# Kernel optimization log

Measured on AMD Instinct MI355X. Metric: run time of the kernel, lower is better.

## Reference

```python
import jax, jax.numpy as jnp
import numpy as np

DIM = 512
NUM_HEADS = 16
RANK = 4
HEAD_DIM = DIM // NUM_HEADS
SCALE = HEAD_DIM ** -0.5
B_, N, NW = 2048, 49, 64


def setup_inputs() -> dict:
    key = jax.random.key(0)
    ks = jax.random.split(key, 9)
    x = jax.random.normal(ks[0], (B_, N, DIM), dtype=jnp.float32)
    mask = jax.random.normal(ks[1], (NW, N, N), dtype=jnp.float32)
    # qkv base linear (torch Linear stores weight [out,in])
    W_qkv = jax.random.normal(ks[2], (3 * DIM, DIM), dtype=jnp.float32) * (DIM ** -0.5)
    b_qkv = jax.random.normal(ks[3], (3 * DIM,), dtype=jnp.float32) * 0.02
    # LoRA down [rank, dim], up [3*dim, rank] (zero-init in module; use small random for non-trivial math)
    A_down = jax.random.normal(ks[4], (RANK, DIM), dtype=jnp.float32) * 0.02
    B_up = jax.random.normal(ks[5], (3 * DIM, RANK), dtype=jnp.float32) * 0.02
    W_proj = jax.random.normal(ks[6], (DIM, DIM), dtype=jnp.float32) * (DIM ** -0.5)
    b_proj = jax.random.normal(ks[7], (DIM,), dtype=jnp.float32) * 0.02
    return {"x": x, "mask": mask, "W_qkv": W_qkv, "b_qkv": b_qkv,
            "A_down": A_down, "B_up": B_up, "W_proj": W_proj, "b_proj": b_proj}


def reference(x, mask, W_qkv, b_qkv, A_down, B_up, W_proj, b_proj):
    Bw, n, C = x.shape
    H, hd = NUM_HEADS, HEAD_DIM
    # LoRA-augmented QKV projection: base linear + up(down(x))
    qkv = x @ W_qkv.T + b_qkv + (x @ A_down.T) @ B_up.T          # [B_, N, 3C]
    qkv = qkv.reshape(Bw, n, 3, H, hd)
    q = qkv[:, :, 0].transpose(0, 2, 1, 3)                        # [B_, H, N, hd]
    k = qkv[:, :, 1].transpose(0, 2, 1, 3)
    v = qkv[:, :, 2].transpose(0, 2, 1, 3)
    attn = jnp.einsum('bhnd,bhmd->bhnm', q, k) * SCALE            # [B_, H, N, N]
    nW = mask.shape[0]
    attn = attn.reshape(Bw // nW, nW, H, n, n) + mask[None, :, None]
    attn = attn.reshape(Bw, H, n, n)
    attn = jax.nn.softmax(attn, axis=-1)
    out = jnp.einsum('bhnm,bhmd->bhnd', attn, v)                  # [B_, H, N, hd]
    out = out.transpose(0, 2, 1, 3).reshape(Bw, n, C)
    return out @ W_proj.T + b_proj
```

## Files before the change

kernel.cpp:

```cpp
#include <hip/hip_runtime.h>
#include <stdint.h>

typedef __attribute__((ext_vector_type(4))) float f32x4;
typedef __attribute__((ext_vector_type(8))) __bf16 bf16x8;
typedef __attribute__((ext_vector_type(4))) unsigned int u32x4;
typedef __attribute__((ext_vector_type(4))) unsigned short u16x4;

#define TOK 49
#define NHEAD 16
#define HDIM 32
#define CDIM 512
#define NB 2048
#define MTOT (NB * TOK)
#define ATT_SCALE 0.17677669529663687f

__device__ __forceinline__ unsigned short f2bf(float f) {
  return __builtin_bit_cast(unsigned short, (__bf16)f);
}

__device__ __forceinline__ void gl_lds16(const void* g, const void* lds) {
  __builtin_amdgcn_global_load_lds(
      (__attribute__((address_space(1))) void*)(uintptr_t)g,
      (__attribute__((address_space(3))) void*)(uint32_t)(uintptr_t)lds,
      16, 0, 0);
}

__device__ __forceinline__ f32x4 mfma16(bf16x8 a, bf16x8 b, f32x4 c) {
  return __builtin_amdgcn_mfma_f32_16x16x32_bf16(a, b, c, 0, 0, 0);
}

__global__ __launch_bounds__(256) void k_prep_weff(
    const float* __restrict__ Wqkv, const float* __restrict__ Bup,
    const float* __restrict__ Adown, unsigned short* __restrict__ weff) {
  int idx = blockIdx.x * 256 + threadIdx.x;
  if (idx >= 3 * CDIM * CDIM) return;
  int o = idx >> 9, i = idx & 511;
  float v = Wqkv[idx];
#pragma unroll
  for (int r = 0; r < 4; r++) v += Bup[o * 4 + r] * Adown[r * 512 + i];
  weff[idx] = f2bf(v);
}

__global__ __launch_bounds__(256) void k_conv4(
    const float* __restrict__ src, unsigned short* __restrict__ dst, int n4) {
  for (int i = blockIdx.x * blockDim.x + threadIdx.x; i < n4;
       i += gridDim.x * blockDim.x) {
    f32x4 v = *(const f32x4*)(src + (size_t)i * 4);
    u16x4 o;
    o[0] = f2bf(v[0]); o[1] = f2bf(v[1]); o[2] = f2bf(v[2]); o[3] = f2bf(v[3]);
    *(u16x4*)(dst + (size_t)i * 4) = o;
  }
}

template <int NT, bool SPLIT>
__global__ __launch_bounds__(256, 2) void k_gemmW(
    const unsigned short* __restrict__ A, const unsigned short* __restrict__ Bw,
    const float* __restrict__ bias,
    unsigned short* __restrict__ qo, unsigned short* __restrict__ ko,
    unsigned short* __restrict__ vo, float* __restrict__ fo) {
  __shared__ __attribute__((aligned(16))) unsigned short smem[36864];
  const int t = threadIdx.x;
  const int l = t & 63;
  const int l15 = l & 15, lq = l >> 4;
  const int w = t >> 6;
  const int wr = w >> 1, wc = w & 1;
  const int bid = blockIdx.x;
  const int lb = (bid & 7) * ((int)gridDim.x >> 3) + (bid >> 3);
  const int mt = lb / NT, nt = lb % NT;
  const size_t m0 = (size_t)mt * 128;
  const int n0 = nt * 256;

  auto stage = [&](int kt, int bb) {
    unsigned short* dA = smem + bb * 4096;
#pragma unroll
    for (int q = 0; q < 2; ++q) {
      const int li = q * 256 + t;
      const int row = li >> 2, sl = li & 3;
      gl_lds16(A + (m0 + row) * CDIM + kt * 32 + ((sl ^ ((row >> 1) & 3)) << 3),
               &dA[li * 8]);
    }
    unsigned short* dB = smem + 12288 + bb * 8192;
#pragma unroll
    for (int q = 0; q < 4; ++q) {
      const int li = q * 256 + t;
      const int row = li >> 2, sl = li & 3;
      gl_lds16(Bw + (size_t)(n0 + row) * CDIM + kt * 32 +
                   ((sl ^ ((row >> 1) & 3)) << 3),
               &dB[li * 8]);
    }
  };

  f32x4 acc[4][8] = {};
  stage(0, 0);
  stage(1, 1);
  for (int kt = 0; kt < 16; ++kt) {
    const int cur = kt % 3;
    if (kt < 15) {
      asm volatile("s_waitcnt vmcnt(6)" ::: "memory");
    } else {
      asm volatile("s_waitcnt vmcnt(0)" ::: "memory");
    }
    __builtin_amdgcn_s_barrier();
    asm volatile("" ::: "memory");
    if (kt < 14) stage(kt + 2, (kt + 2) % 3);
    const unsigned short* bufA = smem + cur * 4096;
    const unsigned short* bufB = smem + 12288 + cur * 8192;
    bf16x8 af[4], bfv[8];
#pragma unroll
    for (int f = 0; f < 4; ++f) {
      const int r = wr * 64 + f * 16 + l15;
      af[f] = __builtin_bit_cast(
          bf16x8, *(const u32x4*)&bufA[r * 32 + ((lq ^ ((r >> 1) & 3)) << 3)]);
    }
#pragma unroll
    for (int c = 0; c < 8; ++c) {
      const int r = wc * 128 + c * 16 + l15;
      bfv[c] = __builtin_bit_cast(
          bf16x8, *(const u32x4*)&bufB[r * 32 + ((lq ^ ((r >> 1) & 3)) << 3)]);
    }
    __builtin_amdgcn_s_setprio(1);
#pragma unroll
    for (int f = 0; f < 4; ++f) {
#pragma unroll
      for (int c = 0; c < 8; ++c) acc[f][c] = mfma16(af[f], bfv[c], acc[f][c]);
    }
    __builtin_amdgcn_s_setprio(0);
    asm volatile("" ::: "memory");
  }

  __syncthreads();
  if constexpr (SPLIT) {
    unsigned short* ep = smem + w * 8192;
#pragma unroll
    for (int J = 0; J < 8; ++J) {
      const int colb = n0 + wc * 128 + J * 16 + l15;
      const float bv = bias[colb];
      const int sl0 = J * 2 + (l15 >> 3);
#pragma unroll
      for (int I = 0; I < 4; ++I) {
#pragma unroll
        for (int r = 0; r < 4; ++r) {
          const int row = I * 16 + lq * 4 + r;
          ep[row * 128 + ((sl0 ^ (row & 7)) << 3) + (l15 & 7)] =
              f2bf(acc[I][J][r] + bv);
        }
      }
    }
    asm volatile("s_waitcnt lgkmcnt(0)" ::: "memory");
    __builtin_amdgcn_s_barrier();
#pragma unroll
    for (int rnd = 0; rnd < 16; ++rnd) {
      const int sub = rnd * 16 + (l >> 2);
      const int mloc = sub >> 2, hd = sub & 3;
      const int colh = n0 + wc * 128 + hd * 32;
      const int which = colh >> 9;
      const int hh = (colh >> 5) & 15;
      unsigned short* dst = which == 0 ? qo : (which == 1 ? ko : vo);
      const uint32_t mg = (uint32_t)(m0 + wr * 64 + mloc);
      const uint32_t bw_ = mg / 49u;
      const uint32_t nn = mg - bw_ * 49u;
      const int slot = hd * 4 + (l & 3);
      u32x4 v = *(const u32x4*)&ep[mloc * 128 + ((slot ^ (mloc & 7)) << 3)];
      *(u32x4*)&dst[((size_t)(bw_ * 16u + hh) * 49u + nn) * 32u + (l & 3) * 8] =
          v;
    }
  } else {
    float* ep32 = (float*)(smem) + w * 4096;
#pragma unroll
    for (int ch = 0; ch < 2; ++ch) {
#pragma unroll
      for (int J2 = 0; J2 < 4; ++J2) {
        const int colb = n0 + wc * 128 + ch * 64 + J2 * 16 + l15;
        const float bv = bias[colb];
        const int sl0 = J2 * 4 + (l15 >> 2);
#pragma unroll
        for (int I = 0; I < 4; ++I) {
#pragma unroll
          for (int r = 0; r < 4; ++r) {
            const int row = I * 16 + lq * 4 + r;
            ep32[row * 64 + ((sl0 ^ (row & 7)) << 2) + (l15 & 3)] =
                acc[I][ch * 4 + J2][r] + bv;
          }
        }
      }
      asm volatile("s_waitcnt lgkmcnt(0)" ::: "memory");
#pragma unroll
      for (int rnd = 0; rnd < 16; ++rnd) {
        const int row = rnd * 4 + (l >> 4);
        const int slot = l & 15;
        f32x4 v = *(const f32x4*)&ep32[row * 64 + ((slot ^ (row & 7)) << 2)];
        const size_t mg = m0 + wr * 64 + row;
        *(f32x4*)&fo[mg * CDIM + n0 + wc * 128 + ch * 64 + (l & 15) * 4] = v;
      }
      asm volatile("s_waitcnt lgkmcnt(0)" ::: "memory");
      asm volatile("" ::: "memory");
    }
  }
}

__global__ __launch_bounds__(256) void k_attn(
    const unsigned short* __restrict__ qb, const unsigned short* __restrict__ kb,
    const unsigned short* __restrict__ vb, const float* __restrict__ mask,
    unsigned short* __restrict__ ao) {
  __shared__ __attribute__((aligned(16))) unsigned short sP[4][64 * 64];
  __shared__ __attribute__((aligned(16))) unsigned short sV[4][32 * 64];
  const int t = threadIdx.x;
  const int l = t & 63, w = t >> 6;
  const int l15 = l & 15, lq = l >> 4;
  const int pair = blockIdx.x * 4 + w;
  const int b = pair >> 4, h = pair & 15;
  const size_t base = (size_t)pair * (TOK * HDIM);
  unsigned short* P = sP[w];
  unsigned short* Vt = sV[w];

  bf16x8 qf[4], kf[4];
#pragma unroll
  for (int i = 0; i < 4; i++)
    qf[i] = __builtin_bit_cast(
        bf16x8, *(const u32x4*)(qb + base + (size_t)(i * 16 + l15) * 32 + lq * 8));
#pragma unroll
  for (int i = 0; i < 4; i++)
    kf[i] = __builtin_bit_cast(
        bf16x8, *(const u32x4*)(kb + base + (size_t)(i * 16 + l15) * 32 + lq * 8));
  u32x4 vr[4];
#pragma unroll
  for (int j = 0; j < 4; j++)
    vr[j] = *(const u32x4*)(vb + base + (size_t)l * 32 + j * 8);

  f32x4 s[4][4];
  __builtin_amdgcn_s_setprio(1);
#pragma unroll
  for (int i = 0; i < 4; i++) {
#pragma unroll
    for (int j = 0; j < 4; j++) s[i][j] = mfma16(qf[i], kf[j], (f32x4)0.0f);
  }
  __builtin_amdgcn_s_setprio(0);

  const bool vok = (l < TOK);
  const int tsl = ((l >> 3) & 7);
  const int tlo = l & 7;
#pragma unroll
  for (int j = 0; j < 4; j++) {
#pragma unroll
    for (int c = 0; c < 4; c++) {
      uint32_t u = vr[j][c];
      int d0 = j * 8 + c * 2;
      Vt[(d0 + 0) * 64 + ((tsl ^ ((d0 + 0) & 7)) << 3) + tlo] =
          vok ? (unsigned short)(u & 0xFFFFu) : (unsigned short)0;
      Vt[(d0 + 1) * 64 + ((tsl ^ ((d0 + 1) & 7)) << 3) + tlo] =
          vok ? (unsigned short)(u >> 16) : (unsigned short)0;
    }
  }

  const float* mrow = mask + (size_t)(b & 63) * (TOK * TOK);
#pragma unroll
  for (int i = 0; i < 4; i++) {
#pragma unroll
    for (int r = 0; r < 4; r++) {
      int row = i * 16 + lq * 4 + r;
#pragma unroll
      for (int j = 0; j < 4; j++) {
        int col = j * 16 + l15;
        float xv = s[i][j][r] * ATT_SCALE;
        if (col < TOK) {
          if (row < TOK) xv += mrow[row * TOK + col];
        } else {
          xv = -1e30f;
        }
        s[i][j][r] = xv;
      }
    }
  }

  float rinv[4][4];
#pragma unroll
  for (int i = 0; i < 4; i++) {
#pragma unroll
    for (int r = 0; r < 4; r++) {
      float m = fmaxf(fmaxf(s[i][0][r], s[i][1][r]), fmaxf(s[i][2][r], s[i][3][r]));
      m = fmaxf(m, __shfl_xor(m, 1));
      m = fmaxf(m, __shfl_xor(m, 2));
      m = fmaxf(m, __shfl_xor(m, 4));
      m = fmaxf(m, __shfl_xor(m, 8));
      float sum = 0.f;
      int row = i * 16 + lq * 4 + r;
#pragma unroll
      for (int j = 0; j < 4; j++) {
        float p = __expf(s[i][j][r] - m);
        sum += p;
        P[row * 64 + (((j * 2 + (l15 >> 3)) ^ (row & 7)) << 3) + (l15 & 7)] =
            f2bf(p);
      }
      sum += __shfl_xor(sum, 1);
      sum += __shfl_xor(sum, 2);
      sum += __shfl_xor(sum, 4);
      sum += __shfl_xor(sum, 8);
      rinv[i][r] = 1.0f / sum;
    }
  }

  asm volatile("s_waitcnt lgkmcnt(0)" ::: "memory");
  __builtin_amdgcn_sched_barrier(0);

  f32x4 o[4][2] = {};
#pragma unroll
  for (int ks = 0; ks < 2; ks++) {
    bf16x8 pa[4], vf[2];
#pragma unroll
    for (int i = 0; i < 4; i++)
      pa[i] = __builtin_bit_cast(
          bf16x8,
          *(const u32x4*)&P[(i * 16 + l15) * 64 + (((lq + ks * 4) ^ (l15 & 7)) << 3)]);
#pragma unroll
    for (int j = 0; j < 2; j++)
      vf[j] = __builtin_bit_cast(
          bf16x8,
          *(const u32x4*)&Vt[(j * 16 + l15) * 64 + (((lq + ks * 4) ^ (l15 & 7)) << 3)]);
    __builtin_amdgcn_s_setprio(1);
#pragma unroll
    for (int i = 0; i < 4; i++) {
#pragma unroll
      for (int j = 0; j < 2; j++) o[i][j] = mfma16(pa[i], vf[j], o[i][j]);
    }
    __builtin_amdgcn_s_setprio(0);
  }

#pragma unroll
  for (int i = 0; i < 4; i++) {
#pragma unroll
    for (int r = 0; r < 4; r++) {
      int row = i * 16 + lq * 4 + r;
      if (row < TOK) {
        float inv = rinv[i][r];
        size_t obase = ((size_t)b * TOK + row) * CDIM + h * HDIM;
#pragma unroll
        for (int j = 0; j < 2; j++)
          ao[obase + j * 16 + l15] = f2bf(o[i][j][r] * inv);
      }
    }
  }
}

extern "C" void kernel_launch(void* const* d_in, const int* in_sizes, int n_in,
                              void* d_out, int out_size, void* d_ws,
                              size_t ws_size, hipStream_t stream) {
  const float* x = (const float*)d_in[0];
  const float* mask = (const float*)d_in[1];
  const float* Wqkv = (const float*)d_in[2];
  const float* bqkv = (const float*)d_in[3];
  const float* Adown = (const float*)d_in[4];
  const float* Bup = (const float*)d_in[5];
  const float* Wproj = (const float*)d_in[6];
  const float* bproj = (const float*)d_in[7];
  float* out = (float*)d_out;
  char* ws = (char*)d_ws;

  size_t off = 0;
  auto alloc = [&](size_t bytes) {
    size_t o = off;
    off += (bytes + 255) & ~(size_t)255;
    return o;
  };
  const size_t qkv_elems = (size_t)NB * NHEAD * TOK * HDIM;
  unsigned short* weff = (unsigned short*)(ws + alloc((size_t)3 * CDIM * CDIM * 2));
  unsigned short* wpb = (unsigned short*)(ws + alloc((size_t)CDIM * CDIM * 2));
  unsigned short* qb = (unsigned short*)(ws + alloc(qkv_elems * 2 + 4096));
  unsigned short* kb = (unsigned short*)(ws + alloc(qkv_elems * 2 + 4096));
  unsigned short* vb = (unsigned short*)(ws + alloc(qkv_elems * 2 + 4096));
  unsigned short* xb = (unsigned short*)(ws + alloc((size_t)MTOT * CDIM * 2));
  unsigned short* ao = xb;

  k_prep_weff<<<(3 * CDIM * CDIM + 255) / 256, 256, 0, stream>>>(Wqkv, Bup,
                                                                 Adown, weff);
  k_conv4<<<256, 256, 0, stream>>>(Wproj, wpb, CDIM * CDIM / 4);
  k_conv4<<<2048, 256, 0, stream>>>(x, xb, MTOT * CDIM / 4);
  k_gemmW<6, true><<<(MTOT / 128) * 6, 256, 0, stream>>>(
      xb, weff, bqkv, qb, kb, vb, nullptr);
  k_attn<<<NB * NHEAD / 4, 256, 0, stream>>>(qb, kb, vb, mask, ao);
  k_gemmW<2, false><<<(MTOT / 128) * 2, 256, 0, stream>>>(
      ao, wpb, bproj, nullptr, nullptr, nullptr, out);
}
```

Before: 541.5 us.

## Fuse fp32-to-bf16 x conversion into QKV GEMM and stage mask in LDS

```diff
diff --git a/kernel.cpp b/kernel.cpp
--- a/kernel.cpp
+++ b/kernel.cpp
@@ -16,6 +16,9 @@
 
 __device__ __forceinline__ unsigned short f2bf(float f) {
   return __builtin_bit_cast(unsigned short, (__bf16)f);
+}
+__device__ __forceinline__ float bf2f(unsigned short u) {
+  return __builtin_bit_cast(float, (uint32_t)u << 16);
 }
 
 __device__ __forceinline__ void gl_lds16(const void* g, const void* lds) {
@@ -52,13 +55,16 @@
   }
 }
 
-template <int NT, bool SPLIT>
-__global__ __launch_bounds__(256, 2) void k_gemmW(
-    const unsigned short* __restrict__ A, const unsigned short* __restrict__ Bw,
+template <int NT, bool SPLIT, bool AF32>
+__global__ __launch_bounds__(256, AF32 ? 1 : 2) void k_gemmW(
+    const void* __restrict__ Ain, const unsigned short* __restrict__ Bw,
     const float* __restrict__ bias,
     unsigned short* __restrict__ qo, unsigned short* __restrict__ ko,
     unsigned short* __restrict__ vo, float* __restrict__ fo) {
-  __shared__ __attribute__((aligned(16))) unsigned short smem[36864];
+  __shared__ __attribute__((aligned(16))) unsigned short smem[AF32 ? 49152
+                                                                   : 36864];
+  const unsigned short* Ab = (const unsigned short*)Ain;
+  const float* Af = (const float*)Ain;
   const int t = threadIdx.x;
   const int l = t & 63;
   const int l15 = l & 15, lq = l >> 4;
@@ -69,17 +75,30 @@
   const int mt = lb / NT, nt = lb % NT;
   const size_t m0 = (size_t)mt * 128;
   const int n0 = nt * 256;
+  constexpr int BOFF = AF32 ? 24576 : 12288;
 
   auto stage = [&](int kt, int bb) {
-    unsigned short* dA = smem + bb * 4096;
-#pragma unroll
-    for (int q = 0; q < 2; ++q) {
-      const int li = q * 256 + t;
-      const int row = li >> 2, sl = li & 3;
-      gl_lds16(A + (m0 + row) * CDIM + kt * 32 + ((sl ^ ((row >> 1) & 3)) << 3),
-               &dA[li * 8]);
-    }
-    unsigned short* dB = smem + 12288 + bb * 8192;
+    if constexpr (AF32) {
+      unsigned short* dA = smem + bb * 8192;
+#pragma unroll
+      for (int q = 0; q < 4; ++q) {
+        const int li = q * 256 + t;
+        const int row = li >> 3, sl = li & 7;
+        gl_lds16(Af + (m0 + row) * CDIM + kt * 32 + ((sl ^ (row & 7)) << 2),
+                 &dA[li * 8]);
+      }
+    } else {
+      unsigned short* dA = smem + bb * 4096;
+#pragma unroll
+      for (int q = 0; q < 2; ++q) {
+        const int li = q * 256 + t;
+        const int row = li >> 2, sl = li & 3;
+        gl_lds16(
+            Ab + (m0 + row) * CDIM + kt * 32 + ((sl ^ ((row >> 1) & 3)) << 3),
+            &dA[li * 8]);
+      }
+    }
+    unsigned short* dB = smem + BOFF + bb * 8192;
 #pragma unroll
     for (int q = 0; q < 4; ++q) {
       const int li = q * 256 + t;
@@ -96,22 +115,43 @@
   for (int kt = 0; kt < 16; ++kt) {
     const int cur = kt % 3;
     if (kt < 15) {
-      asm volatile("s_waitcnt vmcnt(6)" ::: "memory");
+      if constexpr (AF32)
+        asm volatile("s_waitcnt vmcnt(8)" ::: "memory");
+      else
+        asm volatile("s_waitcnt vmcnt(6)" ::: "memory");
     } else {
       asm volatile("s_waitcnt vmcnt(0)" ::: "memory");
     }
     __builtin_amdgcn_s_barrier();
     asm volatile("" ::: "memory");
     if (kt < 14) stage(kt + 2, (kt + 2) % 3);
-    const unsigned short* bufA = smem + cur * 4096;
-    const unsigned short* bufB = smem + 12288 + cur * 8192;
     bf16x8 af[4], bfv[8];
-#pragma unroll
-    for (int f = 0; f < 4; ++f) {
-      const int r = wr * 64 + f * 16 + l15;
-      af[f] = __builtin_bit_cast(
-          bf16x8, *(const u32x4*)&bufA[r * 32 + ((lq ^ ((r >> 1) & 3)) << 3)]);
-    }
+    if constexpr (AF32) {
+      const float* bufAf = (const float*)(smem + cur * 8192);
+#pragma unroll
+      for (int f = 0; f < 4; ++f) {
+        const int r = wr * 64 + f * 16 + l15;
+        const int x7 = r & 7;
+        f32x4 lo = *(const f32x4*)&bufAf[r * 32 + (((2 * lq) ^ x7) << 2)];
+        f32x4 hi = *(const f32x4*)&bufAf[r * 32 + (((2 * lq + 1) ^ x7) << 2)];
+        bf16x8 a;
+        a[0] = (__bf16)lo[0]; a[1] = (__bf16)lo[1];
+        a[2] = (__bf16)lo[2]; a[3] = (__bf16)lo[3];
+        a[4] = (__bf16)hi[0]; a[5] = (__bf16)hi[1];
+        a[6] = (__bf16)hi[2]; a[7] = (__bf16)hi[3];
+        af[f] = a;
+      }
+    } else {
+      const unsigned short* bufA = smem + cur * 4096;
+#pragma unroll
+      for (int f = 0; f < 4; ++f) {
+        const int r = wr * 64 + f * 16 + l15;
+        af[f] = __builtin_bit_cast(
+            bf16x8,
+            *(const u32x4*)&bufA[r * 32 + ((lq ^ ((r >> 1) & 3)) << 3)]);
+      }
+    }
+    const unsigned short* bufB = smem + BOFF + cur * 8192;
 #pragma unroll
     for (int c = 0; c < 8; ++c) {
       const int r = wc * 128 + c * 16 + l15;
@@ -204,14 +244,22 @@
     unsigned short* __restrict__ ao) {
   __shared__ __attribute__((aligned(16))) unsigned short sP[4][64 * 64];
   __shared__ __attribute__((aligned(16))) unsigned short sV[4][32 * 64];
+  __shared__ __attribute__((aligned(16))) unsigned short sM[2432];
   const int t = threadIdx.x;
   const int l = t & 63, w = t >> 6;
   const int l15 = l & 15, lq = l >> 4;
   const int pair = blockIdx.x * 4 + w;
-  const int b = pair >> 4, h = pair & 15;
+  const int h = pair & 15;
+  const int bmask = (blockIdx.x >> 2) & 63;
+  const int b = pair >> 4;
   const size_t base = (size_t)pair * (TOK * HDIM);
   unsigned short* P = sP[w];
   unsigned short* Vt = sV[w];
+
+  {
+    const float* msrc = mask + (size_t)bmask * (TOK * TOK);
+    for (int idx = t; idx < TOK * TOK; idx += 256) sM[idx] = f2bf(msrc[idx]);
+  }
 
   bf16x8 qf[4], kf[4];
 #pragma unroll
@@ -252,7 +300,8 @@
     }
   }
 
-  const float* mrow = mask + (size_t)(b & 63) * (TOK * TOK);
+  __syncthreads();
+
 #pragma unroll
   for (int i = 0; i < 4; i++) {
 #pragma unroll
@@ -263,7 +312,7 @@
         int col = j * 16 + l15;
         float xv = s[i][j][r] * ATT_SCALE;
         if (col < TOK) {
-          if (row < TOK) xv += mrow[row * TOK + col];
+          if (row < TOK) xv += bf2f(sM[row * TOK + col]);
         } else {
           xv = -1e30f;
         }
@@ -367,16 +416,14 @@
   unsigned short* qb = (unsigned short*)(ws + alloc(qkv_elems * 2 + 4096));
   unsigned short* kb = (unsigned short*)(ws + alloc(qkv_elems * 2 + 4096));
   unsigned short* vb = (unsigned short*)(ws + alloc(qkv_elems * 2 + 4096));
-  unsigned short* xb = (unsigned short*)(ws + alloc((size_t)MTOT * CDIM * 2));
-  unsigned short* ao = xb;
+  unsigned short* ao = (unsigned short*)(ws + alloc((size_t)MTOT * CDIM * 2));
 
   k_prep_weff<<<(3 * CDIM * CDIM + 255) / 256, 256, 0, stream>>>(Wqkv, Bup,
                                                                  Adown, weff);
   k_conv4<<<256, 256, 0, stream>>>(Wproj, wpb, CDIM * CDIM / 4);
-  k_conv4<<<2048, 256, 0, stream>>>(x, xb, MTOT * CDIM / 4);
-  k_gemmW<6, true><<<(MTOT / 128) * 6, 256, 0, stream>>>(
-      xb, weff, bqkv, qb, kb, vb, nullptr);
+  k_gemmW<6, true, true><<<(MTOT / 128) * 6, 256, 0, stream>>>(
+      x, weff, bqkv, qb, kb, vb, nullptr);
   k_attn<<<NB * NHEAD / 4, 256, 0, stream>>>(qb, kb, vb, mask, ao);
-  k_gemmW<2, false><<<(MTOT / 128) * 2, 256, 0, stream>>>(
+  k_gemmW<2, false, false><<<(MTOT / 128) * 2, 256, 0, stream>>>(
       ao, wpb, bproj, nullptr, nullptr, nullptr, out);
 }
```

Result: slower. 594.8 us (+9.8%).
